# Kernel tuning notes

Hardware: AMD Instinct MI355X
Metric: run time of the kernel (lower is better)

## Reference

```python
import jax, jax.numpy as jnp
import numpy as np

N_NODES = 50000
N_EDGES = 640000
D_IN, D_HID, D_OUT = 128, 256, 2


def setup_inputs() -> dict:
    key = jax.random.key(0)
    ks = jax.random.split(key, 8)
    node_features = jax.random.normal(ks[0], (N_NODES, D_IN), dtype=jnp.float32)
    src = jax.random.randint(ks[1], (N_EDGES,), 0, N_NODES)
    dst = jax.random.randint(ks[2], (N_EDGES,), 0, N_NODES)
    s_in = 1.0 / np.sqrt(D_IN)
    s_hid = 1.0 / np.sqrt(D_HID)
    return {
        "node_features": node_features,
        "src": src,
        "dst": dst,
        "W1_self": jax.random.normal(ks[3], (D_IN, D_HID), dtype=jnp.float32) * s_in,
        "W1_neigh": jax.random.normal(ks[4], (D_IN, D_HID), dtype=jnp.float32) * s_in,
        "b1": jnp.zeros((D_HID,), dtype=jnp.float32),
        "W2_self": jax.random.normal(ks[5], (D_HID, D_OUT), dtype=jnp.float32) * s_hid,
        "W2_neigh": jax.random.normal(ks[6], (D_HID, D_OUT), dtype=jnp.float32) * s_hid,
        "b2": jnp.zeros((D_OUT,), dtype=jnp.float32),
    }


def _sage_mean(x, src, dst, W_self, W_neigh, b, n_nodes):
    # gather source-node features along edges, mean-reduce into destinations
    msg = x[src]                                                  # [E, D]
    agg = jax.ops.segment_sum(msg, dst, num_segments=n_nodes)     # [N, D]
    deg = jax.ops.segment_sum(jnp.ones((src.shape[0], 1), x.dtype), dst,
                              num_segments=n_nodes)               # [N, 1]
    h_neigh = agg / jnp.maximum(deg, 1.0)
    return x @ W_self + h_neigh @ W_neigh + b


def reference(node_features, src, dst, W1_self, W1_neigh, b1, W2_self, W2_neigh, b2):
    h = _sage_mean(node_features, src, dst, W1_self, W1_neigh, b1, N_NODES)
    h = jax.nn.relu(h)
    logits = _sage_mean(h, src, dst, W2_self, W2_neigh, b2, N_NODES)
    return logits
```

## Files before the change

### kernel.cpp

```cpp
#include <hip/hip_runtime.h>

#define D_IN 128
#define D_HID 256
#define CH 1024
#define MPAD 50048

typedef short bf16x8 __attribute__((ext_vector_type(8)));
typedef float f32x4 __attribute__((ext_vector_type(4)));
typedef unsigned short ushort8 __attribute__((ext_vector_type(8)));

#define AS1 __attribute__((address_space(1)))
#define AS3 __attribute__((address_space(3)))

__device__ __forceinline__ unsigned short f2bf_rne(float x) {
  unsigned int u = __float_as_uint(x);
  unsigned int r = (u + 0x7FFFu + ((u >> 16) & 1u)) >> 16;
  return (unsigned short)r;
}
__device__ __forceinline__ float bf2f(unsigned short b) {
  return __uint_as_float(((unsigned int)b) << 16);
}

__global__ void k_hist(const int* __restrict__ dst, int* __restrict__ deg, int E) {
  int e = blockIdx.x * blockDim.x + threadIdx.x;
  if (e < E) atomicAdd(&deg[dst[e]], 1);
}

__global__ __launch_bounds__(256) void k_csum(const int* __restrict__ deg,
                                              int* __restrict__ csum, int n) {
  __shared__ int ws[4];
  int t = threadIdx.x, lane = t & 63, w = t >> 6;
  int base = blockIdx.x * CH + t * 4;
  int s = 0;
  #pragma unroll
  for (int j = 0; j < 4; ++j) { int i = base + j; s += (i < n) ? deg[i] : 0; }
  #pragma unroll
  for (int off = 32; off > 0; off >>= 1) s += __shfl_down(s, off, 64);
  if (lane == 0) ws[w] = s;
  __syncthreads();
  if (t == 0) csum[blockIdx.x] = ws[0] + ws[1] + ws[2] + ws[3];
}

__global__ void k_coff(const int* __restrict__ csum, int* __restrict__ coff, int nb) {
  int lane = threadIdx.x & 63;
  int v = (lane < nb) ? csum[lane] : 0;
  int x = v;
  #pragma unroll
  for (int off = 1; off < 64; off <<= 1) {
    int u = __shfl_up(x, off, 64);
    if (lane >= off) x += u;
  }
  if (lane < nb) coff[lane] = x - v;
}

__global__ __launch_bounds__(256) void k_scanw(const int* __restrict__ deg,
                                               const int* __restrict__ coff,
                                               int* __restrict__ rs, int n) {
  __shared__ int ws[4];
  int t = threadIdx.x, lane = t & 63, w = t >> 6;
  int base = blockIdx.x * CH + t * 4;
  int d[4];
  #pragma unroll
  for (int j = 0; j < 4; ++j) { int i = base + j; d[j] = (i < n) ? deg[i] : 0; }
  int tt = d[0] + d[1] + d[2] + d[3];
  int x = tt;
  #pragma unroll
  for (int off = 1; off < 64; off <<= 1) {
    int u = __shfl_up(x, off, 64);
    if (lane >= off) x += u;
  }
  if (lane == 63) ws[w] = x;
  __syncthreads();
  if (t == 0) { int s = 0;
    #pragma unroll
    for (int j = 0; j < 4; ++j) { int tmp = ws[j]; ws[j] = s; s += tmp; } }
  __syncthreads();
  int excl = ws[w] + (x - tt) + coff[blockIdx.x];
  #pragma unroll
  for (int j = 0; j < 4; ++j) {
    int i = base + j;
    excl += d[j];
    if (i < n) rs[i + 1] = excl;
  }
  if (blockIdx.x == 0 && t == 0) rs[0] = 0;
}

__global__ void k_scatter(const int* __restrict__ src, const int* __restrict__ dst,
                          const int* __restrict__ rs, int* __restrict__ cursor,
                          int* __restrict__ esrc, int E) {
  int e = blockIdx.x * blockDim.x + threadIdx.x;
  if (e < E) {
    int d = dst[e];
    int pos = rs[d] + atomicAdd(&cursor[d], 1);
    esrc[pos] = src[e];
  }
}

__global__ __launch_bounds__(256) void k_convW(const float* __restrict__ W1s,
                                               const float* __restrict__ W1n,
                                               unsigned short* __restrict__ Bth,
                                               unsigned short* __restrict__ Btl) {
  int k = blockIdx.x;
  int col = threadIdx.x;
  float w = (k < 128) ? W1s[(size_t)k * D_HID + col]
                      : W1n[(size_t)(k - 128) * D_HID + col];
  unsigned short hi = f2bf_rne(w);
  unsigned short lo = f2bf_rne(w - bf2f(hi));
  Bth[(size_t)col * 256 + k] = hi;
  Btl[(size_t)col * 256 + k] = lo;
}

__global__ void k_agg1(const float* __restrict__ X, const int* __restrict__ rs,
                       const int* __restrict__ esrc,
                       unsigned short* __restrict__ Mh,
                       unsigned short* __restrict__ Ml, int n) {
  int wid = (blockIdx.x * blockDim.x + threadIdx.x) >> 6;
  int lane = threadIdx.x & 63;
  if (wid >= n) return;
  int s0 = rs[wid], s1 = rs[wid + 1];
  float ax0 = 0.f, ay0 = 0.f, ax1 = 0.f, ay1 = 0.f;
  int e = s0;
  for (; e + 3 < s1; e += 4) {
    int i0 = esrc[e + 0], i1 = esrc[e + 1], i2 = esrc[e + 2], i3 = esrc[e + 3];
    float2 v0 = *(const float2*)(X + (size_t)i0 * D_IN + lane * 2);
    float2 v1 = *(const float2*)(X + (size_t)i1 * D_IN + lane * 2);
    float2 v2 = *(const float2*)(X + (size_t)i2 * D_IN + lane * 2);
    float2 v3 = *(const float2*)(X + (size_t)i3 * D_IN + lane * 2);
    ax0 += v0.x; ay0 += v0.y;
    ax1 += v1.x; ay1 += v1.y;
    ax0 += v2.x; ay0 += v2.y;
    ax1 += v3.x; ay1 += v3.y;
  }
  for (; e < s1; ++e) {
    int s = esrc[e];
    float2 v = *(const float2*)(X + (size_t)s * D_IN + lane * 2);
    ax0 += v.x; ay0 += v.y;
  }
  int d = s1 - s0;
  float inv = 1.0f / (float)(d > 1 ? d : 1);
  float mx = (ax0 + ax1) * inv, my = (ay0 + ay1) * inv;
  unsigned short hx = f2bf_rne(mx), hy = f2bf_rne(my);
  unsigned short lx = f2bf_rne(mx - bf2f(hx)), ly = f2bf_rne(my - bf2f(hy));
  *(ushort2*)(Mh + (size_t)wid * 128 + lane * 2) = make_ushort2(hx, hy);
  *(ushort2*)(Ml + (size_t)wid * 128 + lane * 2) = make_ushort2(lx, ly);
}

__global__ __launch_bounds__(256, 3) void k_gemm1(
    const float* __restrict__ X,
    const unsigned short* __restrict__ Mh, const unsigned short* __restrict__ Ml,
    const unsigned short* __restrict__ Bth, const unsigned short* __restrict__ Btl,
    const float* __restrict__ b1, const float* __restrict__ W2s,
    const float* __restrict__ W2n, float* __restrict__ SP, int n) {
  __shared__ __align__(16) unsigned short sAh[4][512];
  __shared__ __align__(16) unsigned short sAl[4][512];
  __shared__ __align__(16) unsigned short sBh[16][512];
  __shared__ __align__(16) unsigned short sBl[16][512];

  const int tid = threadIdx.x;
  const int w = tid >> 6;
  const int l = tid & 63;
  const int c = l & 15;
  const int g = l >> 4;
  const int m0 = blockIdx.x * 64;

  f32x4 acc[16];
  #pragma unroll
  for (int i = 0; i < 16; ++i) acc[i] = (f32x4)0.f;

  const int arow = m0 + w * 16 + c;
  const int xrow = (arow < n) ? arow : (n - 1);

  for (int ks = 0; ks < 8; ++ks) {
    const int kt = ks * 32;
    if (kt < 128) {
      const float* src = X + (size_t)xrow * D_IN + kt + g * 8;
      float4 u0 = *(const float4*)(src);
      float4 u1 = *(const float4*)(src + 4);
      float v[8] = {u0.x, u0.y, u0.z, u0.w, u1.x, u1.y, u1.z, u1.w};
      ushort8 hh, ll;
      #pragma unroll
      for (int i = 0; i < 8; ++i) {
        unsigned short h = f2bf_rne(v[i]);
        hh[i] = h;
        ll[i] = f2bf_rne(v[i] - bf2f(h));
      }
      *(ushort8*)(&sAh[w][l * 8]) = hh;
      *(ushort8*)(&sAl[w][l * 8]) = ll;
    } else {
      const unsigned short* mh = Mh + (size_t)arow * 128 + (kt - 128) + g * 8;
      const unsigned short* ml = Ml + (size_t)arow * 128 + (kt - 128) + g * 8;
      __builtin_amdgcn_global_load_lds((AS1 const void*)mh, (AS3 void*)&sAh[w][0], 16, 0, 0);
      __builtin_amdgcn_global_load_lds((AS1 const void*)ml, (AS3 void*)&sAl[w][0], 16, 0, 0);
    }
    #pragma unroll
    for (int q = 0; q < 4; ++q) {
      int ni = w * 4 + q;
      const unsigned short* bh = Bth + (size_t)(ni * 16 + c) * 256 + kt + g * 8;
      const unsigned short* bl = Btl + (size_t)(ni * 16 + c) * 256 + kt + g * 8;
      __builtin_amdgcn_global_load_lds((AS1 const void*)bh, (AS3 void*)&sBh[ni][0], 16, 0, 0);
      __builtin_amdgcn_global_load_lds((AS1 const void*)bl, (AS3 void*)&sBl[ni][0], 16, 0, 0);
    }
    __syncthreads();

    bf16x8 ah = *(const bf16x8*)(&sAh[w][l * 8]);
    bf16x8 al = *(const bf16x8*)(&sAl[w][l * 8]);
    #pragma unroll
    for (int ni = 0; ni < 16; ++ni) {
      bf16x8 bh = *(const bf16x8*)(&sBh[ni][l * 8]);
      bf16x8 bl = *(const bf16x8*)(&sBl[ni][l * 8]);
      acc[ni] = __builtin_amdgcn_mfma_f32_16x16x32_bf16(ah, bh, acc[ni], 0, 0, 0);
      acc[ni] = __builtin_amdgcn_mfma_f32_16x16x32_bf16(ah, bl, acc[ni], 0, 0, 0);
      acc[ni] = __builtin_amdgcn_mfma_f32_16x16x32_bf16(al, bh, acc[ni], 0, 0, 0);
    }
    __syncthreads();
  }

  float s0[4] = {0.f, 0.f, 0.f, 0.f}, s1[4] = {0.f, 0.f, 0.f, 0.f};
  float p0[4] = {0.f, 0.f, 0.f, 0.f}, p1[4] = {0.f, 0.f, 0.f, 0.f};
  #pragma unroll
  for (int ni = 0; ni < 16; ++ni) {
    int col = ni * 16 + c;
    float bb = b1[col];
    float2 ws = *(const float2*)(W2s + (size_t)col * 2);
    float2 wn = *(const float2*)(W2n + (size_t)col * 2);
    #pragma unroll
    for (int j = 0; j < 4; ++j) {
      float h = fmaxf(acc[ni][j] + bb, 0.f);
      s0[j] += h * ws.x; s1[j] += h * ws.y;
      p0[j] += h * wn.x; p1[j] += h * wn.y;
    }
  }
  #pragma unroll
  for (int j = 0; j < 4; ++j) {
    #pragma unroll
    for (int off = 1; off < 16; off <<= 1) {
      s0[j] += __shfl_xor(s0[j], off, 64);
      s1[j] += __shfl_xor(s1[j], off, 64);
      p0[j] += __shfl_xor(p0[j], off, 64);
      p1[j] += __shfl_xor(p1[j], off, 64);
    }
  }
  if (c == 0) {
    #pragma unroll
    for (int j = 0; j < 4; ++j) {
      int row = m0 + w * 16 + g * 4 + j;
      float4 o; o.x = s0[j]; o.y = s1[j]; o.z = p0[j]; o.w = p1[j];
      *(float4*)(SP + (size_t)row * 4) = o;
    }
  }
}

__global__ void k_agg2(const float* __restrict__ SP,
                       const int* __restrict__ rs, const int* __restrict__ esrc,
                       const float* __restrict__ b2,
                       float* __restrict__ out, int n) {
  int nid = blockIdx.x * blockDim.x + threadIdx.x;
  if (nid >= n) return;
  int s0 = rs[nid], s1 = rs[nid + 1];
  float a00 = 0.f, a01 = 0.f, a10 = 0.f, a11 = 0.f;
  int e = s0;
  for (; e + 3 < s1; e += 4) {
    int i0 = esrc[e + 0], i1 = esrc[e + 1], i2 = esrc[e + 2], i3 = esrc[e + 3];
    float2 p0 = *(const float2*)(SP + (size_t)i0 * 4 + 2);
    float2 p1 = *(const float2*)(SP + (size_t)i1 * 4 + 2);
    float2 p2 = *(const float2*)(SP + (size_t)i2 * 4 + 2);
    float2 p3 = *(const float2*)(SP + (size_t)i3 * 4 + 2);
    a00 += p0.x; a01 += p0.y;
    a10 += p1.x; a11 += p1.y;
    a00 += p2.x; a01 += p2.y;
    a10 += p3.x; a11 += p3.y;
  }
  for (; e < s1; ++e) {
    int s = esrc[e];
    float2 p = *(const float2*)(SP + (size_t)s * 4 + 2);
    a00 += p.x; a01 += p.y;
  }
  int d = s1 - s0;
  float inv = 1.0f / (float)(d > 1 ? d : 1);
  float2 sv = *(const float2*)(SP + (size_t)nid * 4);
  float2 o;
  o.x = sv.x + b2[0] + (a00 + a10) * inv;
  o.y = sv.y + b2[1] + (a01 + a11) * inv;
  *(float2*)(out + (size_t)nid * 2) = o;
}

extern "C" void kernel_launch(void* const* d_in, const int* in_sizes, int n_in,
                              void* d_out, int out_size, void* d_ws, size_t ws_size,
                              hipStream_t stream) {
  const float* X   = (const float*)d_in[0];
  const int*   src = (const int*)d_in[1];
  const int*   dst = (const int*)d_in[2];
  const float* W1s = (const float*)d_in[3];
  const float* W1n = (const float*)d_in[4];
  const float* b1  = (const float*)d_in[5];
  const float* W2s = (const float*)d_in[6];
  const float* W2n = (const float*)d_in[7];
  const float* b2  = (const float*)d_in[8];
  float* out = (float*)d_out;

  const int N = in_sizes[0] / D_IN;
  const int E = in_sizes[1];
  const int NB = (N + CH - 1) / CH;

  int* deg    = (int*)d_ws;
  int* cursor = deg + N;
  int* rs     = cursor + N;
  int* csum   = rs + (N + 8);
  int* coff   = csum + 64;
  int* esrc   = coff + 64;
  float* SP   = (float*)(esrc + E);
  unsigned short* Mh  = (unsigned short*)(SP + (size_t)MPAD * 4);
  unsigned short* Ml  = Mh + (size_t)MPAD * 128;
  unsigned short* Bth = Ml + (size_t)MPAD * 128;
  unsigned short* Btl = Bth + 256 * 256;

  hipMemsetAsync(deg, 0, sizeof(int) * (size_t)2 * N, stream);

  int eb = (E + 255) / 256;
  k_convW  <<<256, 256, 0, stream>>>(W1s, W1n, Bth, Btl);
  k_hist   <<<eb, 256, 0, stream>>>(dst, deg, E);
  k_csum   <<<NB, 256, 0, stream>>>(deg, csum, N);
  k_coff   <<<1, 64, 0, stream>>>(csum, coff, NB);
  k_scanw  <<<NB, 256, 0, stream>>>(deg, coff, rs, N);
  k_scatter<<<eb, 256, 0, stream>>>(src, dst, rs, cursor, esrc, E);
  k_agg1   <<<(N + 3) / 4, 256, 0, stream>>>(X, rs, esrc, Mh, Ml, N);
  k_gemm1  <<<MPAD / 64, 256, 0, stream>>>(X, Mh, Ml, Bth, Btl,
                                           b1, W2s, W2n, SP, N);
  k_agg2   <<<(N + 255) / 256, 256, 0, stream>>>(SP, rs, esrc, b2, out, N);
}
```

Before: 255.4 us.

## Switch layer-1 GEMM to 32x32x16 MFMA with 2x2 wave tiling

Reorganizes the fused layer-1 GEMM so each wave computes a 32x128 tile with 32x32x16 bf16 MFMAs instead of a 16x256 strip with 16x16x32 MFMAs. The aim is fewer LDS B-fragment reads per MFMA and better operand reuse. The epilogue now reduces partial layer-2 projections across the two column-half waves through shared memory. The cost is an extra barrier plus cross-wave reduction, and a wider shuffle reduction over 32 lanes.

```diff
diff --git a/kernel.cpp b/kernel.cpp
--- a/kernel.cpp
+++ b/kernel.cpp
@@ -7,6 +7,7 @@
 
 typedef short bf16x8 __attribute__((ext_vector_type(8)));
 typedef float f32x4 __attribute__((ext_vector_type(4)));
+typedef float f32x16 __attribute__((ext_vector_type(16)));
 typedef unsigned short ushort8 __attribute__((ext_vector_type(8)));
 
 #define AS1 __attribute__((address_space(1)))
@@ -151,29 +152,29 @@
     const unsigned short* __restrict__ Bth, const unsigned short* __restrict__ Btl,
     const float* __restrict__ b1, const float* __restrict__ W2s,
     const float* __restrict__ W2n, float* __restrict__ SP, int n) {
-  __shared__ __align__(16) unsigned short sAh[4][512];
-  __shared__ __align__(16) unsigned short sAl[4][512];
-  __shared__ __align__(16) unsigned short sBh[16][512];
-  __shared__ __align__(16) unsigned short sBl[16][512];
+  __shared__ __align__(16) unsigned short sA[2][2][2][512];
+  __shared__ __align__(16) unsigned short sB[8][2][2][512];
 
   const int tid = threadIdx.x;
   const int w = tid >> 6;
   const int l = tid & 63;
-  const int c = l & 15;
-  const int g = l >> 4;
+  const int wm = w & 1, wn = w >> 1;
+  const int r32 = l & 31;
+  const int kh = l >> 5;
   const int m0 = blockIdx.x * 64;
 
-  f32x4 acc[16];
-  #pragma unroll
-  for (int i = 0; i < 16; ++i) acc[i] = (f32x4)0.f;
-
-  const int arow = m0 + w * 16 + c;
+  f32x16 acc[4];
+  #pragma unroll
+  for (int q = 0; q < 4; ++q) acc[q] = (f32x16)0.f;
+
+  const int sm = w & 1, sk = w >> 1;
+  const int arow = m0 + sm * 32 + r32;
   const int xrow = (arow < n) ? arow : (n - 1);
 
   for (int ks = 0; ks < 8; ++ks) {
     const int kt = ks * 32;
     if (kt < 128) {
-      const float* src = X + (size_t)xrow * D_IN + kt + g * 8;
+      const float* src = X + (size_t)xrow * D_IN + kt + sk * 16 + kh * 8;
       float4 u0 = *(const float4*)(src);
       float4 u1 = *(const float4*)(src + 4);
       float v[8] = {u0.x, u0.y, u0.z, u0.w, u1.x, u1.y, u1.z, u1.w};
@@ -184,69 +185,80 @@
         hh[i] = h;
         ll[i] = f2bf_rne(v[i] - bf2f(h));
       }
-      *(ushort8*)(&sAh[w][l * 8]) = hh;
-      *(ushort8*)(&sAl[w][l * 8]) = ll;
+      *(ushort8*)(&sA[sm][sk][0][l * 8]) = hh;
+      *(ushort8*)(&sA[sm][sk][1][l * 8]) = ll;
     } else {
-      const unsigned short* mh = Mh + (size_t)arow * 128 + (kt - 128) + g * 8;
-      const unsigned short* ml = Ml + (size_t)arow * 128 + (kt - 128) + g * 8;
-      __builtin_amdgcn_global_load_lds((AS1 const void*)mh, (AS3 void*)&sAh[w][0], 16, 0, 0);
-      __builtin_amdgcn_global_load_lds((AS1 const void*)ml, (AS3 void*)&sAl[w][0], 16, 0, 0);
-    }
+      const unsigned short* mh = Mh + (size_t)arow * 128 + (kt - 128) + sk * 16 + kh * 8;
+      const unsigned short* ml = Ml + (size_t)arow * 128 + (kt - 128) + sk * 16 + kh * 8;
+      __builtin_amdgcn_global_load_lds((AS1 const void*)mh, (AS3 void*)&sA[sm][sk][0][0], 16, 0, 0);
+      __builtin_amdgcn_global_load_lds((AS1 const void*)ml, (AS3 void*)&sA[sm][sk][1][0], 16, 0, 0);
+    }
+    #pragma unroll
+    for (int q = 0; q < 2; ++q) {
+      int ct = w * 2 + q;
+      #pragma unroll
+      for (int kstep = 0; kstep < 2; ++kstep) {
+        const unsigned short* bh = Bth + (size_t)(ct * 32 + r32) * 256 + kt + kstep * 16 + kh * 8;
+        const unsigned short* bl = Btl + (size_t)(ct * 32 + r32) * 256 + kt + kstep * 16 + kh * 8;
+        __builtin_amdgcn_global_load_lds((AS1 const void*)bh, (AS3 void*)&sB[ct][kstep][0][0], 16, 0, 0);
+        __builtin_amdgcn_global_load_lds((AS1 const void*)bl, (AS3 void*)&sB[ct][kstep][1][0], 16, 0, 0);
+      }
+    }
+    __syncthreads();
+
+    #pragma unroll
+    for (int kstep = 0; kstep < 2; ++kstep) {
+      bf16x8 ah = *(const bf16x8*)(&sA[wm][kstep][0][l * 8]);
+      bf16x8 al = *(const bf16x8*)(&sA[wm][kstep][1][l * 8]);
+      #pragma unroll
+      for (int q = 0; q < 4; ++q) {
+        int ct = wn * 4 + q;
+        bf16x8 bh = *(const bf16x8*)(&sB[ct][kstep][0][l * 8]);
+        bf16x8 bl = *(const bf16x8*)(&sB[ct][kstep][1][l * 8]);
+        acc[q] = __builtin_amdgcn_mfma_f32_32x32x16_bf16(ah, bh, acc[q], 0, 0, 0);
+        acc[q] = __builtin_amdgcn_mfma_f32_32x32x16_bf16(ah, bl, acc[q], 0, 0, 0);
+        acc[q] = __builtin_amdgcn_mfma_f32_32x32x16_bf16(al, bh, acc[q], 0, 0, 0);
+      }
+    }
+    __syncthreads();
+  }
+
+  float b1v[4]; float2 w2sv[4], w2nv[4];
+  #pragma unroll
+  for (int q = 0; q < 4; ++q) {
+    int col = wn * 128 + q * 32 + r32;
+    b1v[q] = b1[col];
+    w2sv[q] = *(const float2*)(W2s + (size_t)col * 2);
+    w2nv[q] = *(const float2*)(W2n + (size_t)col * 2);
+  }
+  float4* fpart = (float4*)&sB[0][0][0][0];
+  #pragma unroll
+  for (int j = 0; j < 16; ++j) {
+    float s0 = 0.f, s1 = 0.f, p0 = 0.f, p1 = 0.f;
     #pragma unroll
     for (int q = 0; q < 4; ++q) {
-      int ni = w * 4 + q;
-      const unsigned short* bh = Bth + (size_t)(ni * 16 + c) * 256 + kt + g * 8;
-      const unsigned short* bl = Btl + (size_t)(ni * 16 + c) * 256 + kt + g * 8;
-      __builtin_amdgcn_global_load_lds((AS1 const void*)bh, (AS3 void*)&sBh[ni][0], 16, 0, 0);
-      __builtin_amdgcn_global_load_lds((AS1 const void*)bl, (AS3 void*)&sBl[ni][0], 16, 0, 0);
-    }
-    __syncthreads();
-
-    bf16x8 ah = *(const bf16x8*)(&sAh[w][l * 8]);
-    bf16x8 al = *(const bf16x8*)(&sAl[w][l * 8]);
-    #pragma unroll
-    for (int ni = 0; ni < 16; ++ni) {
-      bf16x8 bh = *(const bf16x8*)(&sBh[ni][l * 8]);
-      bf16x8 bl = *(const bf16x8*)(&sBl[ni][l * 8]);
-      acc[ni] = __builtin_amdgcn_mfma_f32_16x16x32_bf16(ah, bh, acc[ni], 0, 0, 0);
-      acc[ni] = __builtin_amdgcn_mfma_f32_16x16x32_bf16(ah, bl, acc[ni], 0, 0, 0);
-      acc[ni] = __builtin_amdgcn_mfma_f32_16x16x32_bf16(al, bh, acc[ni], 0, 0, 0);
-    }
-    __syncthreads();
-  }
-
-  float s0[4] = {0.f, 0.f, 0.f, 0.f}, s1[4] = {0.f, 0.f, 0.f, 0.f};
-  float p0[4] = {0.f, 0.f, 0.f, 0.f}, p1[4] = {0.f, 0.f, 0.f, 0.f};
-  #pragma unroll
-  for (int ni = 0; ni < 16; ++ni) {
-    int col = ni * 16 + c;
-    float bb = b1[col];
-    float2 ws = *(const float2*)(W2s + (size_t)col * 2);
-    float2 wn = *(const float2*)(W2n + (size_t)col * 2);
-    #pragma unroll
-    for (int j = 0; j < 4; ++j) {
-      float h = fmaxf(acc[ni][j] + bb, 0.f);
-      s0[j] += h * ws.x; s1[j] += h * ws.y;
-      p0[j] += h * wn.x; p1[j] += h * wn.y;
-    }
-  }
-  #pragma unroll
-  for (int j = 0; j < 4; ++j) {
-    #pragma unroll
-    for (int off = 1; off < 16; off <<= 1) {
-      s0[j] += __shfl_xor(s0[j], off, 64);
-      s1[j] += __shfl_xor(s1[j], off, 64);
-      p0[j] += __shfl_xor(p0[j], off, 64);
-      p1[j] += __shfl_xor(p1[j], off, 64);
-    }
-  }
-  if (c == 0) {
-    #pragma unroll
-    for (int j = 0; j < 4; ++j) {
-      int row = m0 + w * 16 + g * 4 + j;
-      float4 o; o.x = s0[j]; o.y = s1[j]; o.z = p0[j]; o.w = p1[j];
-      *(float4*)(SP + (size_t)row * 4) = o;
-    }
+      float h = fmaxf(acc[q][j] + b1v[q], 0.f);
+      s0 += h * w2sv[q].x; s1 += h * w2sv[q].y;
+      p0 += h * w2nv[q].x; p1 += h * w2nv[q].y;
+    }
+    #pragma unroll
+    for (int off = 1; off < 32; off <<= 1) {
+      s0 += __shfl_xor(s0, off, 64);
+      s1 += __shfl_xor(s1, off, 64);
+      p0 += __shfl_xor(p0, off, 64);
+      p1 += __shfl_xor(p1, off, 64);
+    }
+    if (r32 == 0) {
+      int row = wm * 32 + (j & 3) + 8 * (j >> 2) + 4 * kh;
+      float4 o; o.x = s0; o.y = s1; o.z = p0; o.w = p1;
+      fpart[wn * 64 + row] = o;
+    }
+  }
+  __syncthreads();
+  if (w == 0) {
+    float4 a = fpart[l], b = fpart[64 + l];
+    float4 o; o.x = a.x + b.x; o.y = a.y + b.y; o.z = a.z + b.z; o.w = a.w + b.w;
+    *(float4*)(SP + (size_t)(m0 + l) * 4) = o;
   }
 }
 
```

New measurement: 255.7 us. About the same (+0.1%).
